# Kernel tuning notes

Hardware: AMD Instinct MI355X
Metric: run time of the kernel (lower is better)

## Reference

```python
import jax, jax.numpy as jnp
import numpy as np

INTERVAL = 4
UPSCALE = 4
K = 3              # sample_size
SAMPLERS = 3
Q = 2 ** INTERVAL                 # 16
L = 2 ** (8 - INTERVAL) + 1       # 17
PAD = K - 1
B, H, W = 4, 512, 512

_STRIDES = np.array([L ** 3, L ** 2, L, 1], dtype=np.int32)


def ste_round(x):
    # straight-through round (round_func in the torch code)
    return x + jax.lax.stop_gradient(jnp.round(x) - x)


def fix_weight(w):
    return jnp.clip(ste_round(w * 127.0), -127.0, 127.0)


def sample(img, sw, sb):
    # unfold(K, K-1) + conv-per-patch + fold is exactly a VALID conv.
    # img: (B,1,h+PAD,w+PAD); sw: (4,1,K,K) -> a,b,c,d each (B,1,h,w)
    out = jax.lax.conv_general_dilated(img, sw, (1, 1), 'VALID',
        dimension_numbers=('NCHW', 'OIHW', 'NCHW')) + sb[None, :, None, None]
    return out[:, 0:1], out[:, 1:2], out[:, 2:3], out[:, 3:4]


def interp(lut, res_w, sw, sb, scale, img_in, prev_img):
    # InterpTorchBatch: 4D simplex interpolation into the quantized LUT.
    # Sorted-simplex form is equivalent to the 24-case masked torch code
    # (ties yield zero-weight terms, so tie ordering is irrelevant).
    w = fix_weight(lut)                                       # (L^4, scale*scale)
    a, b, c, d = sample(img_in, sw, sb)
    if prev_img is not None:
        rw = jnp.clip(res_w, 0.0, 1.0)
        pa, pb, pc, pd = sample(prev_img, sw, sb)
        a = rw[0, 0] * pa + (1.0 - rw[0, 0]) * a
        b = rw[0, 1] * pb + (1.0 - rw[0, 1]) * b
        c = rw[1, 0] * pc + (1.0 - rw[1, 0]) * c
        d = rw[1, 1] * pd + (1.0 - rw[1, 1]) * d
    vals = jnp.concatenate([a, b, c, d], axis=1).transpose(0, 2, 3, 1)   # (B,h,w,4)
    lo = jnp.floor_divide(vals, float(Q)).astype(jnp.int32)
    f = jnp.mod(vals, float(Q))
    order = jnp.argsort(-f, axis=-1)                          # fractional parts, descending
    fs = jnp.take_along_axis(f, order, axis=-1)
    strides = jnp.asarray(_STRIDES)
    base = jnp.sum(lo * strides, axis=-1)                     # flat index of p0000
    inc = jnp.cumsum(strides[order], axis=-1)
    verts = jnp.concatenate([base[..., None], base[..., None] + inc], axis=-1)  # (B,h,w,5)
    ws = jnp.concatenate([float(Q) - fs[..., :1], fs[..., :-1] - fs[..., 1:], fs[..., -1:]], axis=-1)
    p = w[verts]                                              # gather: (B,h,w,5,scale*scale)
    out = jnp.einsum('bhwv,bhwvk->bhwk', ws, p) / float(Q)
    bb, hh, ww, _ = out.shape
    out = out.reshape(bb, hh, ww, scale, scale).transpose(0, 1, 3, 2, 4)
    return out.reshape(bb, 1, hh * scale, ww * scale)


def _pad_rot(x, r):
    return jnp.pad(jnp.rot90(x, r, axes=(2, 3)),
                   ((0, 0), (0, 0), (0, PAD), (0, PAD)), mode='edge')


def rotate_input(lut, scale, sw, sb, x, res_w, prev_x):
    pred = jnp.zeros((), jnp.float32)
    for r in range(4):
        pr = None if prev_x is None else _pad_rot(prev_x, r)
        pred = pred + jnp.rot90(
            interp(lut, res_w, sw, sb, scale, _pad_rot(x, r), pr),
            (4 - r) % 4, axes=(2, 3))
        pred = ste_round(pred)
    return pred


def autolut_forward(x, lut0, lut1, samp0, samp1, sbias0, sbias1, resw1):
    x = x * 255.0
    # stage 0: scale 1, no residual, bias 127
    pred = 0.0
    for s in range(SAMPLERS):
        pred = pred + rotate_input(lut0[s], 1, samp0[s], sbias0[s], x, None, None)
    prev_x = x
    x = ste_round(jnp.clip(pred / (SAMPLERS * 4.0) + 127.0, 0.0, 255.0))
    # stage 1 (last): upscale, residual blend with previous stage input
    pred = 0.0
    for s in range(SAMPLERS):
        pred = pred + rotate_input(lut1[s], UPSCALE, samp1[s], sbias1[s], x, resw1[s], prev_x)
    x = ste_round(jnp.clip(pred / float(SAMPLERS), 0.0, 255.0))
    return x / 255.0   # phase == 'train'


def setup_inputs() -> dict:
    key = jax.random.key(0)
    ks = jax.random.split(key, 6)
    x = jax.random.uniform(ks[0], (B, 1, H, W), dtype=jnp.float32)
    lut0 = jax.random.uniform(ks[1], (SAMPLERS, L ** 4, 1), jnp.float32, -1.0, 1.0)
    lut1 = jax.random.uniform(ks[2], (SAMPLERS, L ** 4, UPSCALE * UPSCALE), jnp.float32, -1.0, 1.0)

    def mk_sampler(k):
        w = jax.random.normal(k, (SAMPLERS, 4, 1, K, K), dtype=jnp.float32)
        # convex combination of patch pixels -> sampled values stay in [0,255]
        return jax.nn.softmax(w.reshape(SAMPLERS, 4, -1), axis=-1).reshape(SAMPLERS, 4, 1, K, K)

    samp0 = mk_sampler(ks[3])
    samp1 = mk_sampler(ks[4])
    sbias0 = jnp.zeros((SAMPLERS, 4), jnp.float32)
    sbias1 = jnp.zeros((SAMPLERS, 4), jnp.float32)
    resw1 = jax.random.uniform(ks[5], (SAMPLERS, 2, 2), dtype=jnp.float32)
    return {"x": x, "lut0": lut0, "lut1": lut1, "samp0": samp0, "samp1": samp1,
            "sbias0": sbias0, "sbias1": sbias1, "resw1": resw1}


def reference(x, lut0, lut1, samp0, samp1, sbias0, sbias1, resw1):
    return autolut_forward(x, lut0, lut1, samp0, samp1, sbias0, sbias1, resw1)
```

## Files before the change

kernel.cpp:

```cpp
#include <hip/hip_runtime.h>
#include <math.h>

static constexpr int B_ = 4;
static constexpr int N_ = 512;
static constexpr int N4_ = 2048;
static constexpr int NPIX = B_ * N_ * N_;
static constexpr int LUT_ROWS = 83521;
static constexpr int SPAD = 83584;
static constexpr int ST0 = 4913, ST1 = 289, ST2 = 17, ST3 = 1;
static constexpr int SCHUNK = SPAD / 16;

__device__ __forceinline__ float fixw(float v) {
    v = rintf(v * 127.0f);
    return fminf(fmaxf(v, -127.0f), 127.0f);
}

__global__ void fix_lut0_kernel(const float* __restrict__ in, char* __restrict__ out) {
    int t = blockIdx.x * blockDim.x + threadIdx.x;
    int s = blockIdx.y;
    if (t < LUT_ROWS) out[(size_t)s * SPAD + t] = (char)(int)fixw(in[(size_t)s * LUT_ROWS + t]);
}

__global__ void fix_lut1_kernel(const float4* __restrict__ in, uchar4* __restrict__ out, int n4) {
    int t = blockIdx.x * blockDim.x + threadIdx.x;
    if (t < n4) {
        float4 v = in[t];
        uchar4 o;
        o.x = (unsigned char)((int)fixw(v.x) + 127);
        o.y = (unsigned char)((int)fixw(v.y) + 127);
        o.z = (unsigned char)((int)fixw(v.z) + 127);
        o.w = (unsigned char)((int)fixw(v.w) + 127);
        out[t] = o;
    }
}

struct Simplex {
    int v[5];
    float w[5];
};

__device__ __forceinline__ double pack_key(float f, unsigned stride) {
    unsigned long long u = ((unsigned long long)__float_as_uint(f) << 32) | stride;
    return __longlong_as_double((long long)u);
}
__device__ __forceinline__ float key_f(double k) {
    return __uint_as_float((unsigned)((unsigned long long)__double_as_longlong(k) >> 32));
}
__device__ __forceinline__ int key_s(double k) {
    return (int)(unsigned)__double_as_longlong(k);
}

__device__ __forceinline__ Simplex simplex4(float a, float b, float c, float d) {
    float fl0 = floorf(a * 0.0625f), fl1 = floorf(b * 0.0625f),
          fl2 = floorf(c * 0.0625f), fl3 = floorf(d * 0.0625f);
    float f0 = a - 16.0f * fl0, f1 = b - 16.0f * fl1,
          f2 = c - 16.0f * fl2, f3 = d - 16.0f * fl3;
    int l0 = min(max((int)fl0, 0), 15);
    int l1 = min(max((int)fl1, 0), 15);
    int l2 = min(max((int)fl2, 0), 15);
    int l3 = min(max((int)fl3, 0), 15);
    double k0 = pack_key(f0, (unsigned)ST0);
    double k1 = pack_key(f1, (unsigned)ST1);
    double k2 = pack_key(f2, (unsigned)ST2);
    double k3 = pack_key(f3, (unsigned)ST3);
#define CSWD(X, Y) { double mx_ = fmax(X, Y); Y = fmin(X, Y); X = mx_; }
    CSWD(k0, k1) CSWD(k2, k3) CSWD(k0, k2) CSWD(k1, k3) CSWD(k1, k2)
#undef CSWD
    Simplex s;
    s.v[0] = l0 * ST0 + l1 * ST1 + l2 * ST2 + l3;
    s.v[1] = s.v[0] + key_s(k0);
    s.v[2] = s.v[1] + key_s(k1);
    s.v[3] = s.v[2] + key_s(k2);
    s.v[4] = s.v[3] + key_s(k3);
    float g0 = key_f(k0), g1 = key_f(k1), g2 = key_f(k2), g3 = key_f(k3);
    s.w[0] = (16.0f - g0) * 0.0625f;
    s.w[1] = (g0 - g1) * 0.0625f;
    s.w[2] = (g1 - g2) * 0.0625f;
    s.w[3] = (g2 - g3) * 0.0625f;
    s.w[4] = g3 * 0.0625f;
    return s;
}

__device__ __forceinline__ bool tap_for_r(int r, int a, int c, int& di, int& dj) {
    if (r == 0) { di = a - 2; dj = c - 2; return (a >= 2) && (c >= 2); }
    if (r == 1) { di = 2 - c; dj = a - 2; return (a >= 2) && (c <= 2); }
    if (r == 2) { di = 2 - a; dj = 2 - c; return (a <= 2) && (c <= 2); }
    di = c - 2; dj = 2 - a; return (a <= 2) && (c >= 2);
}

__device__ __forceinline__ void acc4u(unsigned int q, float wv, float* oc) {
    oc[0] = fmaf(wv, (float)(q & 0xffu), oc[0]);
    oc[1] = fmaf(wv, (float)((q >> 8) & 0xffu), oc[1]);
    oc[2] = fmaf(wv, (float)((q >> 16) & 0xffu), oc[2]);
    oc[3] = fmaf(wv, (float)(q >> 24), oc[3]);
}

__global__ __launch_bounds__(1024, 4) void stage0_kernel(
    const float* __restrict__ x,
    const char* __restrict__ lut0q,
    const float* __restrict__ samp0,
    const float* __restrict__ sbias0,
    float* __restrict__ x1)
{
    __shared__ char luts[SPAD];

    int b    = blockIdx.x >> 8;
    int tile = blockIdx.x & 255;
    int i = ((tile >> 4) << 5) + (threadIdx.x >> 5);
    int j = ((tile & 15) << 5) + (threadIdx.x & 31);
    const int tid = threadIdx.x;
    const float* xb = x + (size_t)b * N_ * N_;

    float vals[3][4][4];
    #pragma unroll
    for (int s = 0; s < 3; ++s)
        #pragma unroll
        for (int r = 0; r < 4; ++r)
            #pragma unroll
            for (int ch = 0; ch < 4; ++ch) vals[s][r][ch] = 0.0f;
    #pragma unroll
    for (int a = 0; a < 5; ++a) {
        int ri = min(max(i - 2 + a, 0), N_ - 1);
        const float* row = xb + ri * N_;
        #pragma unroll
        for (int c = 0; c < 5; ++c) {
            int ci = min(max(j - 2 + c, 0), N_ - 1);
            float px = row[ci] * 255.0f;
            #pragma unroll
            for (int r = 0; r < 4; ++r) {
                int di, dj;
                if (tap_for_r(r, a, c, di, dj)) {
                    #pragma unroll
                    for (int s = 0; s < 3; ++s)
                        #pragma unroll
                        for (int ch = 0; ch < 4; ++ch)
                            vals[s][r][ch] += samp0[s * 36 + ch * 9 + di * 3 + dj] * px;
                }
            }
        }
    }

    float pred = 0.0f;
    #pragma unroll
    for (int s = 0; s < 3; ++s) {
        __syncthreads();
        {
            const char* src = lut0q + (size_t)s * SPAD;
            #pragma unroll
            for (int k = 0; k < 5; ++k) {
                int off = (tid + k * 1024) * 16;
                __builtin_amdgcn_global_load_lds(
                    (const __attribute__((address_space(1))) void*)(src + off),
                    (__attribute__((address_space(3))) void*)(luts + off),
                    16, 0, 0);
            }
            if (tid < SCHUNK - 5120) {
                int off = (tid + 5120) * 16;
                __builtin_amdgcn_global_load_lds(
                    (const __attribute__((address_space(1))) void*)(src + off),
                    (__attribute__((address_space(3))) void*)(luts + off),
                    16, 0, 0);
            }
        }
        __syncthreads();

        const float* sb = sbias0 + s * 4;
        Simplex sx[4];
        #pragma unroll
        for (int r = 0; r < 4; ++r)
            sx[r] = simplex4(vals[s][r][0] + sb[0], vals[s][r][1] + sb[1],
                             vals[s][r][2] + sb[2], vals[s][r][3] + sb[3]);

        float p[4][5];
        #pragma unroll
        for (int r = 0; r < 4; ++r)
            #pragma unroll
            for (int v = 0; v < 5; ++v)
                p[r][v] = (float)luts[sx[r].v[v]];

        float acc = 0.0f;
        #pragma unroll
        for (int r = 0; r < 4; ++r) {
            asm volatile("" : "+v"(p[r][0]), "+v"(p[r][1]), "+v"(p[r][2]),
                              "+v"(p[r][3]), "+v"(p[r][4]));
            float o = sx[r].w[0] * p[r][0] + sx[r].w[1] * p[r][1]
                    + sx[r].w[2] * p[r][2] + sx[r].w[3] * p[r][3]
                    + sx[r].w[4] * p[r][4];
            acc = rintf(acc + o);
        }
        pred += acc;
    }
    x1[(size_t)b * N_ * N_ + i * N_ + j] =
        rintf(fminf(fmaxf(pred / 12.0f + 127.0f, 0.0f), 255.0f));
}

__global__ __launch_bounds__(256, 1) void stage1_kernel(
    const float* __restrict__ x,
    const float* __restrict__ x1,
    const unsigned char* __restrict__ lut1q,
    const float* __restrict__ samp1,
    const float* __restrict__ sbias1,
    const float* __restrict__ resw1,
    float* __restrict__ out)
{
    int b    = blockIdx.x >> 10;
    int tile = blockIdx.x & 1023;
    int i = ((tile >> 5) << 4) + (threadIdx.x >> 4);
    int j = ((tile & 31) << 4) + (threadIdx.x & 15);
    const float* xb  = x  + (size_t)b * N_ * N_;
    const float* x1b = x1 + (size_t)b * N_ * N_;

    float tot[16];
    #pragma unroll
    for (int k = 0; k < 16; ++k) tot[k] = 0.0f;

    for (int s = 0; s < 3; ++s) {
        const float* w  = samp1 + s * 36;
        const unsigned char* lut = lut1q + (size_t)s * LUT_ROWS * 16;
        float rws[4];
        #pragma unroll
        for (int ch = 0; ch < 4; ++ch)
            rws[ch] = fminf(fmaxf(resw1[s * 4 + ch], 0.0f), 1.0f);

        float vals[4][4];
        #pragma unroll
        for (int r = 0; r < 4; ++r)
            #pragma unroll
            for (int ch = 0; ch < 4; ++ch) vals[r][ch] = sbias1[s * 4 + ch];

        #pragma unroll
        for (int a = 0; a < 5; ++a) {
            int ri = min(max(i - 2 + a, 0), N_ - 1);
            const float* r1 = x1b + ri * N_;
            const float* r0 = xb + ri * N_;
            #pragma unroll
            for (int c = 0; c < 5; ++c) {
                int ci = min(max(j - 2 + c, 0), N_ - 1);
                float pc = r1[ci];
                float dq = r0[ci] * 255.0f - pc;
                float q[4];
                #pragma unroll
                for (int ch = 0; ch < 4; ++ch)
                    q[ch] = fmaf(rws[ch], dq, pc);
                #pragma unroll
                for (int r = 0; r < 4; ++r) {
                    int di, dj;
                    if (tap_for_r(r, a, c, di, dj)) {
                        #pragma unroll
                        for (int ch = 0; ch < 4; ++ch)
                            vals[r][ch] += w[ch * 9 + di * 3 + dj] * q[ch];
                    }
                }
            }
        }

        Simplex sx[4];
        #pragma unroll
        for (int r = 0; r < 4; ++r)
            sx[r] = simplex4(vals[r][0], vals[r][1], vals[r][2], vals[r][3]);

        uint4 g[4][5];
        #pragma unroll
        for (int r = 0; r < 4; ++r)
            #pragma unroll
            for (int v = 0; v < 5; ++v)
                g[r][v] = *(const uint4*)(lut + (size_t)sx[r].v[v] * 16);

        float acc[16];
        #pragma unroll
        for (int k = 0; k < 16; ++k) acc[k] = 0.0f;

        #pragma unroll
        for (int r = 0; r < 4; ++r) {
            #pragma unroll
            for (int v = 0; v < 5; ++v)
                asm volatile("" : "+v"(g[r][v].x), "+v"(g[r][v].y),
                                  "+v"(g[r][v].z), "+v"(g[r][v].w));
            float oc[16];
            #pragma unroll
            for (int k = 0; k < 16; ++k) oc[k] = 0.0f;
            #pragma unroll
            for (int v = 0; v < 5; ++v) {
                float wv = sx[r].w[v];
                acc4u(g[r][v].x, wv, oc);
                acc4u(g[r][v].y, wv, oc + 4);
                acc4u(g[r][v].z, wv, oc + 8);
                acc4u(g[r][v].w, wv, oc + 12);
            }
            float S = sx[r].w[0] + sx[r].w[1] + sx[r].w[2] + sx[r].w[3] + sx[r].w[4];
            float bias = 127.0f * S;
            #pragma unroll
            for (int k = 0; k < 16; ++k) oc[k] -= bias;
            #pragma unroll
            for (int u = 0; u < 4; ++u)
                #pragma unroll
                for (int v2 = 0; v2 < 4; ++v2) {
                    int k = 4 * u + v2;
                    int c = (r == 0) ? (4 * u + v2)
                          : (r == 1) ? (4 * (3 - v2) + u)
                          : (r == 2) ? (4 * (3 - u) + (3 - v2))
                                     : (4 * v2 + (3 - u));
                    acc[k] = rintf(acc[k] + oc[c]);
                }
        }
        #pragma unroll
        for (int k = 0; k < 16; ++k) tot[k] += acc[k];
    }

    float* ob = out + (size_t)b * N4_ * N4_ + (size_t)(i * 4) * N4_ + (j * 4);
    #pragma unroll
    for (int u = 0; u < 4; ++u) {
        float4 val;
        val.x = rintf(fminf(fmaxf(tot[4 * u + 0] / 3.0f, 0.0f), 255.0f)) * (1.0f / 255.0f);
        val.y = rintf(fminf(fmaxf(tot[4 * u + 1] / 3.0f, 0.0f), 255.0f)) * (1.0f / 255.0f);
        val.z = rintf(fminf(fmaxf(tot[4 * u + 2] / 3.0f, 0.0f), 255.0f)) * (1.0f / 255.0f);
        val.w = rintf(fminf(fmaxf(tot[4 * u + 3] / 3.0f, 0.0f), 255.0f)) * (1.0f / 255.0f);
        *(float4*)(ob + (size_t)u * N4_) = val;
    }
}

extern "C" void kernel_launch(void* const* d_in, const int* in_sizes, int n_in,
                              void* d_out, int out_size, void* d_ws, size_t ws_size,
                              hipStream_t stream) {
    const float* x      = (const float*)d_in[0];
    const float* lut0   = (const float*)d_in[1];
    const float* lut1   = (const float*)d_in[2];
    const float* samp0  = (const float*)d_in[3];
    const float* samp1  = (const float*)d_in[4];
    const float* sbias0 = (const float*)d_in[5];
    const float* sbias1 = (const float*)d_in[6];
    const float* resw1  = (const float*)d_in[7];
    float* out = (float*)d_out;
    char* ws   = (char*)d_ws;

    const int N_L1 = 3 * LUT_ROWS * 16;
    size_t off_x1 = 0;
    size_t off_l0 = (size_t)NPIX * sizeof(float);
    size_t off_l1 = (off_l0 + (size_t)3 * SPAD + 15) & ~(size_t)15;

    float* x1 = (float*)(ws + off_x1);
    char* l0q = ws + off_l0;
    unsigned char* l1q = (unsigned char*)(ws + off_l1);

    const int threads = 256;

    dim3 g0((LUT_ROWS + threads - 1) / threads, 3);
    fix_lut0_kernel<<<g0, threads, 0, stream>>>(lut0, l0q);
    fix_lut1_kernel<<<(N_L1 / 4 + threads - 1) / threads, threads, 0, stream>>>(
        (const float4*)lut1, (uchar4*)l1q, N_L1 / 4);
    stage0_kernel<<<NPIX / 1024, 1024, 0, stream>>>(x, l0q, samp0, sbias0, x1);
    stage1_kernel<<<NPIX / threads, threads, 0, stream>>>(x, x1, l1q, samp1, sbias1, resw1, out);
}
```

Before: 273.9 us.

## Process four 32x32 tiles per stage0 block to amortize LUT loads to LDS

Stage0 now launches 256 blocks instead of 1024, and each block covers a 64x64 region as four 32x32 sub-tiles. Each quantized LUT0 sampler table is copied into shared memory once per block and reused for four pixels per thread, cutting the total global-to-LDS traffic by four. The sampling convolution is recomputed per sampler inside the loop rather than stored for all three samplers up front, which lowers register pressure but repeats the pixel loads three times. With 256 blocks on 256 CUs each CU gets one block, so there is less parallelism available to hide latency.

```diff
diff --git a/kernel.cpp b/kernel.cpp
--- a/kernel.cpp
+++ b/kernel.cpp
@@ -104,44 +104,17 @@
 {
     __shared__ char luts[SPAD];
 
-    int b    = blockIdx.x >> 8;
-    int tile = blockIdx.x & 255;
-    int i = ((tile >> 4) << 5) + (threadIdx.x >> 5);
-    int j = ((tile & 15) << 5) + (threadIdx.x & 31);
+    int b   = blockIdx.x >> 6;
+    int reg = blockIdx.x & 63;
+    int i0 = (reg >> 3) << 6;
+    int j0 = (reg & 7) << 6;
+    int ti = threadIdx.x >> 5;
+    int tj = threadIdx.x & 31;
     const int tid = threadIdx.x;
     const float* xb = x + (size_t)b * N_ * N_;
 
-    float vals[3][4][4];
-    #pragma unroll
-    for (int s = 0; s < 3; ++s)
-        #pragma unroll
-        for (int r = 0; r < 4; ++r)
-            #pragma unroll
-            for (int ch = 0; ch < 4; ++ch) vals[s][r][ch] = 0.0f;
-    #pragma unroll
-    for (int a = 0; a < 5; ++a) {
-        int ri = min(max(i - 2 + a, 0), N_ - 1);
-        const float* row = xb + ri * N_;
-        #pragma unroll
-        for (int c = 0; c < 5; ++c) {
-            int ci = min(max(j - 2 + c, 0), N_ - 1);
-            float px = row[ci] * 255.0f;
-            #pragma unroll
-            for (int r = 0; r < 4; ++r) {
-                int di, dj;
-                if (tap_for_r(r, a, c, di, dj)) {
-                    #pragma unroll
-                    for (int s = 0; s < 3; ++s)
-                        #pragma unroll
-                        for (int ch = 0; ch < 4; ++ch)
-                            vals[s][r][ch] += samp0[s * 36 + ch * 9 + di * 3 + dj] * px;
-                }
-            }
-        }
-    }
-
-    float pred = 0.0f;
-    #pragma unroll
+    float pred[4] = { 0.0f, 0.0f, 0.0f, 0.0f };
+
     for (int s = 0; s < 3; ++s) {
         __syncthreads();
         {
@@ -165,33 +138,72 @@
         __syncthreads();
 
         const float* sb = sbias0 + s * 4;
-        Simplex sx[4];
-        #pragma unroll
-        for (int r = 0; r < 4; ++r)
-            sx[r] = simplex4(vals[s][r][0] + sb[0], vals[s][r][1] + sb[1],
-                             vals[s][r][2] + sb[2], vals[s][r][3] + sb[3]);
-
-        float p[4][5];
-        #pragma unroll
-        for (int r = 0; r < 4; ++r)
-            #pragma unroll
-            for (int v = 0; v < 5; ++v)
-                p[r][v] = (float)luts[sx[r].v[v]];
-
-        float acc = 0.0f;
-        #pragma unroll
-        for (int r = 0; r < 4; ++r) {
-            asm volatile("" : "+v"(p[r][0]), "+v"(p[r][1]), "+v"(p[r][2]),
-                              "+v"(p[r][3]), "+v"(p[r][4]));
-            float o = sx[r].w[0] * p[r][0] + sx[r].w[1] * p[r][1]
-                    + sx[r].w[2] * p[r][2] + sx[r].w[3] * p[r][3]
-                    + sx[r].w[4] * p[r][4];
-            acc = rintf(acc + o);
+        const float* w  = samp0 + s * 36;
+
+        #pragma unroll
+        for (int t = 0; t < 4; ++t) {
+            int i = i0 + ((t >> 1) << 5) + ti;
+            int j = j0 + ((t & 1) << 5) + tj;
+
+            float vals[4][4];
+            #pragma unroll
+            for (int r = 0; r < 4; ++r)
+                #pragma unroll
+                for (int ch = 0; ch < 4; ++ch) vals[r][ch] = 0.0f;
+            #pragma unroll
+            for (int a = 0; a < 5; ++a) {
+                int ri = min(max(i - 2 + a, 0), N_ - 1);
+                const float* row = xb + ri * N_;
+                #pragma unroll
+                for (int c = 0; c < 5; ++c) {
+                    int ci = min(max(j - 2 + c, 0), N_ - 1);
+                    float px = row[ci] * 255.0f;
+                    #pragma unroll
+                    for (int r = 0; r < 4; ++r) {
+                        int di, dj;
+                        if (tap_for_r(r, a, c, di, dj)) {
+                            #pragma unroll
+                            for (int ch = 0; ch < 4; ++ch)
+                                vals[r][ch] += w[ch * 9 + di * 3 + dj] * px;
+                        }
+                    }
+                }
+            }
+
+            Simplex sx[4];
+            #pragma unroll
+            for (int r = 0; r < 4; ++r)
+                sx[r] = simplex4(vals[r][0] + sb[0], vals[r][1] + sb[1],
+                                 vals[r][2] + sb[2], vals[r][3] + sb[3]);
+
+            float p[4][5];
+            #pragma unroll
+            for (int r = 0; r < 4; ++r)
+                #pragma unroll
+                for (int v = 0; v < 5; ++v)
+                    p[r][v] = (float)luts[sx[r].v[v]];
+
+            float acc = 0.0f;
+            #pragma unroll
+            for (int r = 0; r < 4; ++r) {
+                asm volatile("" : "+v"(p[r][0]), "+v"(p[r][1]), "+v"(p[r][2]),
+                                  "+v"(p[r][3]), "+v"(p[r][4]));
+                float o = sx[r].w[0] * p[r][0] + sx[r].w[1] * p[r][1]
+                        + sx[r].w[2] * p[r][2] + sx[r].w[3] * p[r][3]
+                        + sx[r].w[4] * p[r][4];
+                acc = rintf(acc + o);
+            }
+            pred[t] += acc;
         }
-        pred += acc;
-    }
-    x1[(size_t)b * N_ * N_ + i * N_ + j] =
-        rintf(fminf(fmaxf(pred / 12.0f + 127.0f, 0.0f), 255.0f));
+    }
+
+    #pragma unroll
+    for (int t = 0; t < 4; ++t) {
+        int i = i0 + ((t >> 1) << 5) + ti;
+        int j = j0 + ((t & 1) << 5) + tj;
+        x1[(size_t)b * N_ * N_ + i * N_ + j] =
+            rintf(fminf(fmaxf(pred[t] / 12.0f + 127.0f, 0.0f), 255.0f));
+    }
 }
 
 __global__ __launch_bounds__(256, 1) void stage1_kernel(
@@ -348,6 +360,6 @@
     fix_lut0_kernel<<<g0, threads, 0, stream>>>(lut0, l0q);
     fix_lut1_kernel<<<(N_L1 / 4 + threads - 1) / threads, threads, 0, stream>>>(
         (const float4*)lut1, (uchar4*)l1q, N_L1 / 4);
-    stage0_kernel<<<NPIX / 1024, 1024, 0, stream>>>(x, l0q, samp0, sbias0, x1);
+    stage0_kernel<<<256, 1024, 0, stream>>>(x, l0q, samp0, sbias0, x1);
     stage1_kernel<<<NPIX / threads, threads, 0, stream>>>(x, x1, l1q, samp1, sbias1, resw1, out);
 }
```

After: 323.8 us. 1.18x slower.
